# Kernel tuning notes

Measured on AMD Instinct MI355X. Metric: run time of the kernel, lower is better.

The kernel has to match this reference:

```python
import jax, jax.numpy as jnp
import numpy as np

N_NODES = 50000
N_GRAPHS = 250
NODES_PER_GRAPH = 200
EDGES_PER_GRAPH = 3200  # avg degree 16
F_IN = 128
EMB = 128
HID = 128
VOCAB = 1000
N_REL = 8


def setup_inputs() -> dict:
    key = jax.random.key(0)
    ks = jax.random.split(key, 16)

    # message: col 0 = discrete token id (stored as float), col 1 = continuous value
    disc = jax.random.randint(ks[0], (N_GRAPHS,), 0, VOCAB).astype(jnp.float32)
    cont = jax.random.normal(ks[1], (N_GRAPHS,), dtype=jnp.float32)
    message = jnp.stack([disc, cont], axis=1)  # [B, 2]

    x = jax.random.normal(ks[2], (N_NODES, F_IN), dtype=jnp.float32)

    # within-graph edges: local indices + per-graph node offset
    offs = (jnp.arange(N_GRAPHS, dtype=jnp.int64) * NODES_PER_GRAPH)[:, None]
    src = (jax.random.randint(ks[3], (N_GRAPHS, EDGES_PER_GRAPH), 0, NODES_PER_GRAPH) + offs).reshape(-1)
    dst = (jax.random.randint(ks[4], (N_GRAPHS, EDGES_PER_GRAPH), 0, NODES_PER_GRAPH) + offs).reshape(-1)
    edge_index = jnp.stack([src, dst], axis=0).astype(jnp.int64)  # [2, E]
    edge_type = jax.random.randint(ks[5], (N_GRAPHS * EDGES_PER_GRAPH,), 0, N_REL).astype(jnp.int64)

    batch = jnp.repeat(jnp.arange(N_GRAPHS, dtype=jnp.int64), NODES_PER_GRAPH)  # [N]

    s = 0.05
    W1 = jax.random.normal(ks[6], (N_REL, F_IN, EMB), dtype=jnp.float32) * s
    root1 = jax.random.normal(ks[7], (F_IN, EMB), dtype=jnp.float32) * s
    b1 = jnp.zeros((EMB,), dtype=jnp.float32)
    W2 = jax.random.normal(ks[8], (N_REL, EMB, EMB), dtype=jnp.float32) * s
    root2 = jax.random.normal(ks[9], (EMB, EMB), dtype=jnp.float32) * s
    b2 = jnp.zeros((EMB,), dtype=jnp.float32)
    embed_table = jax.random.normal(ks[10], (VOCAB, EMB), dtype=jnp.float32) * s
    cont_w = jax.random.normal(ks[11], (1, EMB), dtype=jnp.float32) * s
    cont_b = jnp.zeros((EMB,), dtype=jnp.float32)
    msg_w = jax.random.normal(ks[12], (2 * EMB, HID), dtype=jnp.float32) * s
    msg_b = jnp.zeros((HID,), dtype=jnp.float32)

    return {
        "message": message, "x": x, "edge_index": edge_index, "edge_type": edge_type,
        "batch": batch, "max_nodes": NODES_PER_GRAPH,
        "W1": W1, "root1": root1, "b1": b1, "W2": W2, "root2": root2, "b2": b2,
        "embed_table": embed_table, "cont_w": cont_w, "cont_b": cont_b,
        "msg_w": msg_w, "msg_b": msg_b,
    }


def _rgcn_conv(h, src, dst, edge_type, W, root, b, n_nodes, n_rel):
    # per-node per-relation transform, then gather per edge: avoids [E,F,F] weight gather
    hW = jnp.einsum('nf,rfo->nro', h, W)          # [N, R, O]
    msg = hW[src, edge_type]                       # [E, O]
    # mean aggregation per (dst, relation) as in PyG RGCNConv(aggr='mean')
    key_dr = dst * n_rel + edge_type
    cnt = jax.ops.segment_sum(jnp.ones_like(edge_type, dtype=h.dtype), key_dr,
                              num_segments=n_nodes * n_rel)
    norm = 1.0 / jnp.maximum(cnt[key_dr], 1.0)     # [E]
    agg = jax.ops.segment_sum(msg * norm[:, None], dst, num_segments=n_nodes)  # [N, O]
    return agg + h @ root + b


def reference(message, x, edge_index, edge_type, batch, max_nodes,
              W1, root1, b1, W2, root2, b2,
              embed_table, cont_w, cont_b, msg_w, msg_b):
    n_nodes = x.shape[0]
    n_rel = W1.shape[0]
    n_graphs = message.shape[0]
    src, dst = edge_index[0], edge_index[1]

    # --- RGCN node embeddings (2 layers, ReLU between) ---
    h = _rgcn_conv(x, src, dst, edge_type, W1, root1, b1, n_nodes, n_rel)
    h = jax.nn.relu(h)
    node_emb = _rgcn_conv(h, src, dst, edge_type, W2, root2, b2, n_nodes, n_rel)  # [N, EMB]

    # --- message representation ---
    disc_tok = message[:, 0].astype(jnp.int32)
    disc_emb = embed_table[disc_tok]                                   # [B, EMB]
    cont_emb = jax.nn.relu(message[:, 1:2] @ cont_w + cont_b)          # [B, EMB]
    combined = jnp.concatenate([disc_emb, cont_emb], axis=1)           # [B, 2*EMB]
    message_repr = jax.nn.relu(combined @ msg_w + msg_b)               # [B, HID]

    # --- per-node dot score against its graph's message, padded per graph ---
    scores = jnp.einsum('ne,ne->n', node_emb, message_repr[batch])     # [N]
    counts = jax.ops.segment_sum(jnp.ones((n_nodes,), dtype=jnp.int32), batch,
                                 num_segments=n_graphs)
    start = jnp.cumsum(counts) - counts                                # exclusive cumsum
    pos = jnp.arange(n_nodes) - start[batch]                           # slot within graph
    logits = jnp.full((n_graphs, max_nodes), -jnp.inf, dtype=scores.dtype)
    logits = logits.at[batch, pos].set(scores)
    return logits
```

## Files before the change

### kernel.cpp

```cpp
#include <hip/hip_runtime.h>
#include <stdint.h>

#define G_   250
#define P_   200
#define EPG  3200
#define E_   800000
#define F_   128
#define R_   8
#define HROW 136
#define NKEY (R_ * P_)
#define BSTG (8 * 4 * 64 * 8)

typedef _Float16 f16x8 __attribute__((ext_vector_type(8)));
typedef _Float16 f16x4 __attribute__((ext_vector_type(4)));
typedef float    f32x4 __attribute__((ext_vector_type(4)));
typedef float    f32x16 __attribute__((ext_vector_type(16)));

__global__ __launch_bounds__(256) void k_wstage(const float* __restrict__ W1, const float* __restrict__ root1,
                                                const float* __restrict__ W2, const float* __restrict__ root2,
                                                _Float16* __restrict__ wf) {
  int t = blockIdx.x * 256 + threadIdx.x;
  int j    = t & 7;
  int lane = (t >> 3) & 63;
  int ntj  = (t >> 9) & 3;
  int kt   = (t >> 11) & 7;
  int rl_  = t >> 14;
  int r = rl_ % 9, l = rl_ / 9;
  const float* Wl = (l == 0) ? W1 : W2;
  const float* rt = (l == 0) ? root1 : root2;
  int k = kt * 16 + (lane >> 5) * 8 + j;
  int n = ntj * 32 + (lane & 31);
  float v = (r < 8) ? Wl[(r * F_ + k) * F_ + n] : rt[k * F_ + n];
  wf[t] = (_Float16)v;
}

__global__ __launch_bounds__(1024, 4) void k_main(
    const float* __restrict__ x, const int* __restrict__ ei, const int* __restrict__ et,
    const _Float16* __restrict__ wf, const float* __restrict__ b1, const float* __restrict__ b2,
    const float* __restrict__ message, const float* __restrict__ embed,
    const float* __restrict__ cw, const float* __restrict__ cb,
    const float* __restrict__ mw, const float* __restrict__ mb,
    float* __restrict__ out) {
  __shared__ __attribute__((aligned(16))) _Float16 hbuf0[P_ * HROW];
  __shared__ __attribute__((aligned(16))) _Float16 hbuf1[P_ * HROW];
  __shared__ __attribute__((aligned(16))) _Float16 Bstage[BSTG];
  __shared__ unsigned short csrS[EPG];
  __shared__ int offsS[NKEY + 1];
  __shared__ float msgS[F_ + 1];
  __shared__ float scoreS[2 * P_];

  int g = blockIdx.x, tid = threadIdx.x;
  int lane = tid & 63, wave = tid >> 6;
  int m32 = lane & 31, kh = lane >> 5;

  int*   Sint = (int*)hbuf1;
  int*   cnt  = Sint;
  int*   cur  = Sint + 1600;
  int*   eRec = Sint + 3200;
  float* comb = (float*)(Sint + 6400);
  float* red  = (float*)(Sint + 6656);

  f16x8 st0[2];
  st0[0] = *((const f16x8*)(wf + tid * 8));
  st0[1] = *((const f16x8*)(wf + 8192 + tid * 8));

  for (int i = tid; i < P_ * 32; i += 1024) {
    int row = i >> 5, c4 = i & 31;
    const float4 v = ((const float4*)x)[(g * P_ + row) * 32 + c4];
    f16x4 pk = { (_Float16)v.x, (_Float16)v.y, (_Float16)v.z, (_Float16)v.w };
    *((f16x4*)&hbuf0[row * HROW + c4 * 4]) = pk;
  }
  for (int i = tid; i < NKEY; i += 1024) { cnt[i] = 0; cur[i] = 0; }
  if (tid < F_) {
    int tok = (int)message[g * 2];
    float cont = message[g * 2 + 1];
    comb[tid] = embed[tok * F_ + tid];
    float ce = cont * cw[tid] + cb[tid];
    comb[F_ + tid] = ce > 0.0f ? ce : 0.0f;
  }
  *((f16x8*)(Bstage + tid * 8)) = st0[0];
  *((f16x8*)(Bstage + 8192 + tid * 8)) = st0[1];
  __syncthreads();

  int base = g * EPG, nbase = g * P_;
  if (wave == 12 || wave == 13) {
    int col = tid & 127;
    float acc = 0.0f;
#pragma unroll 16
    for (int k2 = 0; k2 < 256; k2++) acc += comb[k2] * mw[k2 * F_ + col];
    red[col] = acc;
  } else {
    int iw = (wave < 12) ? wave : (wave - 2);
    for (int e = iw * 64 + lane; e < EPG; e += 896) {
      int s = ei[base + e] - nbase;
      int d = ei[E_ + base + e] - nbase;
      int r = et[base + e];
      eRec[e] = s | (d << 8) | (r << 16);
      atomicAdd(&cnt[r * P_ + d], 1);
    }
  }
  __syncthreads();

  if (wave == 0) {
    int4 vv[8];
    int osum = 0;
    if (lane < 50) {
      const int4* cp = (const int4*)(cnt + lane * 32);
#pragma unroll
      for (int i = 0; i < 8; i++) { vv[i] = cp[i]; osum += vv[i].x + vv[i].y + vv[i].z + vv[i].w; }
    }
    int incl = osum;
#pragma unroll
    for (int d = 1; d < 64; d <<= 1) {
      int t2 = __shfl_up(incl, d, 64);
      if (lane >= d) incl += t2;
    }
    int run = incl - osum;
    if (lane < 50) {
#pragma unroll
      for (int i = 0; i < 8; i++) {
        offsS[lane * 32 + i * 4 + 0] = run; run += vv[i].x;
        offsS[lane * 32 + i * 4 + 1] = run; run += vv[i].y;
        offsS[lane * 32 + i * 4 + 2] = run; run += vv[i].z;
        offsS[lane * 32 + i * 4 + 3] = run; run += vv[i].w;
      }
    }
    if (lane == 0) offsS[NKEY] = EPG;
  } else if (wave == 1) {
    float m0 = mb[lane] + red[lane];
    float m1 = mb[lane + 64] + red[lane + 64];
    m0 = m0 > 0.0f ? m0 : 0.0f;
    m1 = m1 > 0.0f ? m1 : 0.0f;
    msgS[lane] = m0; msgS[lane + 64] = m1;
    float p = m0 * b2[lane] + m1 * b2[lane + 64];
#pragma unroll
    for (int d = 32; d > 0; d >>= 1) p += __shfl_xor(p, d, 64);
    if (lane == 0) msgS[F_] = p;
  }
  __syncthreads();

  for (int e = tid; e < EPG; e += 1024) {
    int rec = eRec[e];
    int s = rec & 255, d = (rec >> 8) & 255, r = rec >> 16;
    int key = r * P_ + d;
    int pos = atomicAdd(&cur[key], 1);
    csrS[offsS[key] + pos] = (unsigned short)s;
  }
  __syncthreads();

  int rh = wave >> 1, ch = wave & 1;
  int jobBase = rh * 25;
  bool rowAct = (m32 < 25);
  int myD = jobBase + m32;
  int ck = kh * 8;
  int ntB = ch * 2;

  for (int l = 0; l < 2; l++) {
    const _Float16* Ap = (l == 0) ? hbuf0 : hbuf1;
    _Float16* balt = (l == 0) ? hbuf1 : hbuf0;
    f32x16 acc[2];
#pragma unroll
    for (int nt = 0; nt < 2; nt++)
#pragma unroll
      for (int i = 0; i < 16; i++) acc[nt][i] = 0.0f;
    const _Float16* wl = wf + l * (9 * BSTG);
    for (int r = 0; r < 9; r++) {
      f16x8 st2[2];
      bool haveNext = (r < 8) || (l == 0);
      if (haveNext) {
        const _Float16* wnext = (r < 8) ? (wl + (r + 1) * BSTG) : (wf + 9 * BSTG);
        st2[0] = *((const f16x8*)(wnext + tid * 8));
        st2[1] = *((const f16x8*)(wnext + 8192 + tid * 8));
      }
      f16x8 a[8];
      if (r < 8) {
        int o = 0, n = 0;
        if (rowAct) { int key = r * P_ + myD; o = offsS[key]; n = offsS[key + 1] - o; }
        f16x8 z = {0, 0, 0, 0, 0, 0, 0, 0};
#pragma unroll
        for (int kt = 0; kt < 8; kt++) a[kt] = z;
        for (int t = 0; t < n; t++) {
          int s0 = (int)csrS[o + t];
          const _Float16* hp0 = &Ap[s0 * HROW + ck];
#pragma unroll
          for (int kt = 0; kt < 8; kt++) a[kt] += *((const f16x8*)(hp0 + kt * 16));
        }
        float nf = (n > 0) ? 1.0f / (float)n : 0.0f;
        _Float16 nh = (_Float16)nf;
#pragma unroll
        for (int kt = 0; kt < 8; kt++) a[kt] *= nh;
      } else {
        int rowA = jobBase + (rowAct ? m32 : 24);
        const _Float16* hp = &Ap[rowA * HROW + ck];
#pragma unroll
        for (int kt = 0; kt < 8; kt++) a[kt] = *((const f16x8*)(hp + kt * 16));
      }
      const _Float16* bp = (r & 1) ? balt : Bstage;
#pragma unroll
      for (int kt = 0; kt < 8; kt++) {
#pragma unroll
        for (int ntl = 0; ntl < 2; ntl++) {
          f16x8 b = *((const f16x8*)&bp[((kt * 4 + ntB + ntl) * 64 + lane) * 8]);
          acc[ntl] = __builtin_amdgcn_mfma_f32_32x32x16_f16(a[kt], b, acc[ntl], 0, 0, 0);
        }
      }
      if (r < 8) {
        _Float16* dst = ((r + 1) & 1) ? balt : Bstage;
        *((f16x8*)(dst + tid * 8)) = st2[0];
        *((f16x8*)(dst + 8192 + tid * 8)) = st2[1];
        __syncthreads();
      } else if (l == 0) {
        __syncthreads();
        *((f16x8*)(Bstage + tid * 8)) = st2[0];
        *((f16x8*)(Bstage + 8192 + tid * 8)) = st2[1];
      }
    }
    if (l == 0) {
#pragma unroll
      for (int ntl = 0; ntl < 2; ntl++) {
        int col = (ntB + ntl) * 32 + m32;
        float bias = b1[col];
#pragma unroll
        for (int reg = 0; reg < 16; reg++) {
          int row = (reg & 3) + 8 * (reg >> 2) + 4 * kh;
          if (row < 25) {
            float v = acc[ntl][reg] + bias;
            v = v > 0.0f ? v : 0.0f;
            hbuf1[(jobBase + row) * HROW + col] = (_Float16)v;
          }
        }
      }
      __syncthreads();
    } else {
      float mg0 = msgS[ntB * 32 + m32];
      float mg1 = msgS[(ntB + 1) * 32 + m32];
#pragma unroll
      for (int reg = 0; reg < 16; reg++) {
        int row = (reg & 3) + 8 * (reg >> 2) + 4 * kh;
        float p = acc[0][reg] * mg0 + acc[1][reg] * mg1;
        p += __shfl_xor(p, 16, 32);
        p += __shfl_xor(p, 8, 32);
        p += __shfl_xor(p, 4, 32);
        p += __shfl_xor(p, 2, 32);
        p += __shfl_xor(p, 1, 32);
        if (m32 == 0 && row < 25)
          scoreS[ch * P_ + jobBase + row] = p;
      }
      __syncthreads();
      if (tid < P_)
        out[g * P_ + tid] = scoreS[tid] + scoreS[P_ + tid] + msgS[F_];
    }
  }
}

extern "C" void kernel_launch(void* const* d_in, const int* in_sizes, int n_in,
                              void* d_out, int out_size, void* d_ws, size_t ws_size,
                              hipStream_t stream) {
  const float* message = (const float*)d_in[0];
  const float* x       = (const float*)d_in[1];
  const int*   ei      = (const int*)d_in[2];
  const int*   et      = (const int*)d_in[3];
  const float* W1      = (const float*)d_in[6];
  const float* root1   = (const float*)d_in[7];
  const float* b1      = (const float*)d_in[8];
  const float* W2      = (const float*)d_in[9];
  const float* root2   = (const float*)d_in[10];
  const float* b2      = (const float*)d_in[11];
  const float* embed   = (const float*)d_in[12];
  const float* cw      = (const float*)d_in[13];
  const float* cb      = (const float*)d_in[14];
  const float* mw      = (const float*)d_in[15];
  const float* mb      = (const float*)d_in[16];

  _Float16* wfrag = (_Float16*)d_ws;
  float*    out   = (float*)d_out;

  hipLaunchKernelGGL(k_wstage, dim3(1152), dim3(256), 0, stream, W1, root1, W2, root2, wfrag);
  hipLaunchKernelGGL(k_main, dim3(G_), dim3(1024), 0, stream, x, ei, et, wfrag, b1, b2,
                     message, embed, cw, cb, mw, mb, out);
}
```

Before: 184.2 us.

## Split MFMA work along K instead of N to halve redundant neighbor gathers

Waves now split the 128-wide reduction dimension into two halves rather than splitting output columns, so each wave gathers and averages only 64 feature columns per neighbor instead of all 128. Before, each pair of waves gathered the same full rows. Each wave now computes all 4 output tiles, and the two K-halves are summed through shared memory in a staged, multi-barrier epilogue for layer 1. MFMA sections are also wrapped in s_setprio, and the launch-bounds occupancy hint is dropped. The cost is more accumulator registers per wave and extra barriers and LDS traffic in the layer-1 reduction.

```diff
diff --git a/kernel.cpp b/kernel.cpp
--- a/kernel.cpp
+++ b/kernel.cpp
@@ -34,7 +34,28 @@
   wf[t] = (_Float16)v;
 }
 
-__global__ __launch_bounds__(1024, 4) void k_main(
+__device__ __forceinline__ void gather4(f16x8 (&a)[4], const _Float16* __restrict__ Ap,
+                                        const unsigned short* __restrict__ csr,
+                                        const int* __restrict__ offs,
+                                        int key, bool act, int cbck) {
+  int o = 0, n = 0;
+  if (act) { o = offs[key]; n = offs[key + 1] - o; }
+  f16x8 z = {0, 0, 0, 0, 0, 0, 0, 0};
+#pragma unroll
+  for (int kt = 0; kt < 4; kt++) a[kt] = z;
+  for (int t = 0; t < n; t++) {
+    int s0 = (int)csr[o + t];
+    const _Float16* hp = &Ap[s0 * HROW + cbck];
+#pragma unroll
+    for (int kt = 0; kt < 4; kt++) a[kt] += *((const f16x8*)(hp + kt * 16));
+  }
+  float nf = (n > 0) ? 1.0f / (float)n : 0.0f;
+  _Float16 nh = (_Float16)nf;
+#pragma unroll
+  for (int kt = 0; kt < 4; kt++) a[kt] *= nh;
+}
+
+__global__ __launch_bounds__(1024) void k_main(
     const float* __restrict__ x, const int* __restrict__ ei, const int* __restrict__ et,
     const _Float16* __restrict__ wf, const float* __restrict__ b1, const float* __restrict__ b2,
     const float* __restrict__ message, const float* __restrict__ embed,
@@ -60,9 +81,8 @@
   float* comb = (float*)(Sint + 6400);
   float* red  = (float*)(Sint + 6656);
 
-  f16x8 st0[2];
-  st0[0] = *((const f16x8*)(wf + tid * 8));
-  st0[1] = *((const f16x8*)(wf + 8192 + tid * 8));
+  f16x8 st0a = *((const f16x8*)(wf + tid * 8));
+  f16x8 st0b = *((const f16x8*)(wf + 8192 + tid * 8));
 
   for (int i = tid; i < P_ * 32; i += 1024) {
     int row = i >> 5, c4 = i & 31;
@@ -78,8 +98,8 @@
     float ce = cont * cw[tid] + cb[tid];
     comb[F_ + tid] = ce > 0.0f ? ce : 0.0f;
   }
-  *((f16x8*)(Bstage + tid * 8)) = st0[0];
-  *((f16x8*)(Bstage + 8192 + tid * 8)) = st0[1];
+  *((f16x8*)(Bstage + tid * 8)) = st0a;
+  *((f16x8*)(Bstage + 8192 + tid * 8)) = st0b;
   __syncthreads();
 
   int base = g * EPG, nbase = g * P_;
@@ -148,107 +168,147 @@
   }
   __syncthreads();
 
-  int rh = wave >> 1, ch = wave & 1;
-  int jobBase = rh * 25;
+  int H = wave >> 3;
+  int t8 = wave & 7;
+  int jobBase = t8 * 25;
   bool rowAct = (m32 < 25);
   int myD = jobBase + m32;
-  int ck = kh * 8;
-  int ntB = ch * 2;
+  int cbck = H * 64 + kh * 8;
+  int ktBase = H * 4;
+  int rowA = jobBase + (rowAct ? m32 : 24);
 
   for (int l = 0; l < 2; l++) {
     const _Float16* Ap = (l == 0) ? hbuf0 : hbuf1;
     _Float16* balt = (l == 0) ? hbuf1 : hbuf0;
-    f32x16 acc[2];
-#pragma unroll
-    for (int nt = 0; nt < 2; nt++)
+    f32x16 acc[4];
+#pragma unroll
+    for (int nt = 0; nt < 4; nt++)
 #pragma unroll
       for (int i = 0; i < 16; i++) acc[nt][i] = 0.0f;
     const _Float16* wl = wf + l * (9 * BSTG);
+
     for (int r = 0; r < 9; r++) {
-      f16x8 st2[2];
+      f16x8 sta, stb;
       bool haveNext = (r < 8) || (l == 0);
       if (haveNext) {
-        const _Float16* wnext = (r < 8) ? (wl + (r + 1) * BSTG) : (wf + 9 * BSTG);
-        st2[0] = *((const f16x8*)(wnext + tid * 8));
-        st2[1] = *((const f16x8*)(wnext + 8192 + tid * 8));
-      }
-      f16x8 a[8];
+        const _Float16* wn = (r < 8) ? (wl + (r + 1) * BSTG) : (wf + 9 * BSTG);
+        sta = *((const f16x8*)(wn + tid * 8));
+        stb = *((const f16x8*)(wn + 8192 + tid * 8));
+      }
+      f16x8 a[4];
       if (r < 8) {
-        int o = 0, n = 0;
-        if (rowAct) { int key = r * P_ + myD; o = offsS[key]; n = offsS[key + 1] - o; }
-        f16x8 z = {0, 0, 0, 0, 0, 0, 0, 0};
-#pragma unroll
-        for (int kt = 0; kt < 8; kt++) a[kt] = z;
-        for (int t = 0; t < n; t++) {
-          int s0 = (int)csrS[o + t];
-          const _Float16* hp0 = &Ap[s0 * HROW + ck];
-#pragma unroll
-          for (int kt = 0; kt < 8; kt++) a[kt] += *((const f16x8*)(hp0 + kt * 16));
-        }
-        float nf = (n > 0) ? 1.0f / (float)n : 0.0f;
-        _Float16 nh = (_Float16)nf;
-#pragma unroll
-        for (int kt = 0; kt < 8; kt++) a[kt] *= nh;
+        gather4(a, Ap, csrS, offsS, r * P_ + myD, rowAct, cbck);
       } else {
-        int rowA = jobBase + (rowAct ? m32 : 24);
-        const _Float16* hp = &Ap[rowA * HROW + ck];
-#pragma unroll
-        for (int kt = 0; kt < 8; kt++) a[kt] = *((const f16x8*)(hp + kt * 16));
+        const _Float16* hp = &Ap[rowA * HROW + cbck];
+#pragma unroll
+        for (int kt = 0; kt < 4; kt++) a[kt] = *((const f16x8*)(hp + kt * 16));
       }
       const _Float16* bp = (r & 1) ? balt : Bstage;
-#pragma unroll
-      for (int kt = 0; kt < 8; kt++) {
-#pragma unroll
-        for (int ntl = 0; ntl < 2; ntl++) {
-          f16x8 b = *((const f16x8*)&bp[((kt * 4 + ntB + ntl) * 64 + lane) * 8]);
-          acc[ntl] = __builtin_amdgcn_mfma_f32_32x32x16_f16(a[kt], b, acc[ntl], 0, 0, 0);
-        }
-      }
+      __builtin_amdgcn_s_setprio(1);
+#pragma unroll
+      for (int kt = 0; kt < 4; kt++) {
+#pragma unroll
+        for (int nt = 0; nt < 4; nt++) {
+          f16x8 b = *((const f16x8*)&bp[(((ktBase + kt) * 4 + nt) * 64 + lane) * 8]);
+          acc[nt] = __builtin_amdgcn_mfma_f32_32x32x16_f16(a[kt], b, acc[nt], 0, 0, 0);
+        }
+      }
+      __builtin_amdgcn_s_setprio(0);
       if (r < 8) {
-        _Float16* dst = ((r + 1) & 1) ? balt : Bstage;
-        *((f16x8*)(dst + tid * 8)) = st2[0];
-        *((f16x8*)(dst + 8192 + tid * 8)) = st2[1];
+        _Float16* dst = (r & 1) ? Bstage : balt;
+        *((f16x8*)(dst + tid * 8)) = sta;
+        *((f16x8*)(dst + 8192 + tid * 8)) = stb;
         __syncthreads();
-      } else if (l == 0) {
+      } else {
         __syncthreads();
-        *((f16x8*)(Bstage + tid * 8)) = st2[0];
-        *((f16x8*)(Bstage + 8192 + tid * 8)) = st2[1];
-      }
-    }
+        if (l == 0) {
+          *((f16x8*)(Bstage + tid * 8)) = sta;
+          *((f16x8*)(Bstage + 8192 + tid * 8)) = stb;
+        }
+      }
+    }
+
     if (l == 0) {
-#pragma unroll
-      for (int ntl = 0; ntl < 2; ntl++) {
-        int col = (ntB + ntl) * 32 + m32;
-        float bias = b1[col];
-#pragma unroll
-        for (int reg = 0; reg < 16; reg++) {
-          int row = (reg & 3) + 8 * (reg >> 2) + 4 * kh;
-          if (row < 25) {
-            float v = acc[ntl][reg] + bias;
-            v = v > 0.0f ? v : 0.0f;
-            hbuf1[(jobBase + row) * HROW + col] = (_Float16)v;
+      float* c32 = (float*)hbuf0;
+      int slot = t8 & 3;
+      if (wave < 4) {
+#pragma unroll
+        for (int nt = 0; nt < 4; nt++) {
+          int col = nt * 32 + m32;
+#pragma unroll
+          for (int reg = 0; reg < 16; reg++) {
+            int row = (reg & 3) + 8 * (reg >> 2) + 4 * kh;
+            if (row < 25) c32[slot * 3200 + row * 128 + col] = acc[nt][reg];
           }
         }
       }
       __syncthreads();
+      if (wave >= 8 && wave < 12) {
+#pragma unroll
+        for (int nt = 0; nt < 4; nt++) {
+          int col = nt * 32 + m32;
+          float bias = b1[col];
+#pragma unroll
+          for (int reg = 0; reg < 16; reg++) {
+            int row = (reg & 3) + 8 * (reg >> 2) + 4 * kh;
+            if (row < 25) {
+              float v = c32[slot * 3200 + row * 128 + col] + acc[nt][reg] + bias;
+              v = v > 0.0f ? v : 0.0f;
+              hbuf1[(jobBase + row) * HROW + col] = (_Float16)v;
+            }
+          }
+        }
+      }
+      __syncthreads();
+      if (wave >= 4 && wave < 8) {
+#pragma unroll
+        for (int nt = 0; nt < 4; nt++) {
+          int col = nt * 32 + m32;
+#pragma unroll
+          for (int reg = 0; reg < 16; reg++) {
+            int row = (reg & 3) + 8 * (reg >> 2) + 4 * kh;
+            if (row < 25) c32[slot * 3200 + row * 128 + col] = acc[nt][reg];
+          }
+        }
+      }
+      __syncthreads();
+      if (wave >= 12) {
+#pragma unroll
+        for (int nt = 0; nt < 4; nt++) {
+          int col = nt * 32 + m32;
+          float bias = b1[col];
+#pragma unroll
+          for (int reg = 0; reg < 16; reg++) {
+            int row = (reg & 3) + 8 * (reg >> 2) + 4 * kh;
+            if (row < 25) {
+              float v = c32[slot * 3200 + row * 128 + col] + acc[nt][reg] + bias;
+              v = v > 0.0f ? v : 0.0f;
+              hbuf1[(jobBase + row) * HROW + col] = (_Float16)v;
+            }
+          }
+        }
+      }
+      __syncthreads();
     } else {
-      float mg0 = msgS[ntB * 32 + m32];
-      float mg1 = msgS[(ntB + 1) * 32 + m32];
+      float db2 = msgS[F_];
 #pragma unroll
       for (int reg = 0; reg < 16; reg++) {
         int row = (reg & 3) + 8 * (reg >> 2) + 4 * kh;
-        float p = acc[0][reg] * mg0 + acc[1][reg] * mg1;
+        float p = 0.0f;
+#pragma unroll
+        for (int nt = 0; nt < 4; nt++)
+          p += acc[nt][reg] * msgS[nt * 32 + m32];
         p += __shfl_xor(p, 16, 32);
         p += __shfl_xor(p, 8, 32);
         p += __shfl_xor(p, 4, 32);
         p += __shfl_xor(p, 2, 32);
         p += __shfl_xor(p, 1, 32);
         if (m32 == 0 && row < 25)
-          scoreS[ch * P_ + jobBase + row] = p;
+          scoreS[H * P_ + jobBase + row] = p;
       }
       __syncthreads();
       if (tid < P_)
-        out[g * P_ + tid] = scoreS[tid] + scoreS[P_ + tid] + msgS[F_];
+        out[g * P_ + tid] = scoreS[tid] + scoreS[P_ + tid] + db2;
     }
   }
 }
```

Result: no change. 180.7 us (-1.9%).
